# Kernel optimization log

Hardware: AMD Instinct MI355X
Metric: run time of the kernel (lower is better)

## Reference

```python
import jax, jax.numpy as jnp
import numpy as np

B, CIN, HID, T, W, H, TAU = 8, 16, 64, 4, 32, 32, 5
EPS = 1e-5
DN = ('NCDHW', 'OIDHW', 'NCDHW')


def conv3d(x, w, b):
    # 'same' conv3d, NCDHW layout
    y = jax.lax.conv_general_dilated(x, w, (1, 1, 1), 'SAME', dimension_numbers=DN)
    return y + b[None, :, None, None, None]


def ln3(u):
    # F.layer_norm over the last 3 (spatial) dims, no affine
    mu = jnp.mean(u, axis=(-3, -2, -1), keepdims=True)
    var = jnp.var(u, axis=(-3, -2, -1), keepdims=True)
    return (u - mu) * jax.lax.rsqrt(var + EPS)


def ln4(u, w, b):
    # nn.LayerNorm(memory_shape): over last 4 dims (C,T,W,H), with affine
    mu = jnp.mean(u, axis=(-4, -3, -2, -1), keepdims=True)
    var = jnp.var(u, axis=(-4, -3, -2, -1), keepdims=True)
    return (u - mu) * jax.lax.rsqrt(var + EPS) * w + b


def self_attention(r, c_history):
    scale = 1.0 / np.sqrt(T * W * H)
    scores = jnp.einsum('bctwh,lbctwh->bl', r, c_history) * scale  # [B, TAU]
    # faithful to source: softmax over dim=0 (the batch axis of the [b,l] scores)
    attn = jax.nn.softmax(scores, axis=0)
    return jnp.einsum('bl,lbctwh->bctwh', attn, c_history)


def setup_inputs() -> dict:
    key = jax.random.key(0)
    ks = jax.random.split(key, 8)
    x = jax.random.normal(ks[0], (B, CIN, T, W, H), jnp.float32)
    c_history = jax.random.normal(ks[1], (TAU, B, HID, T, W, H), jnp.float32)
    m = jax.random.normal(ks[2], (B, HID, T, W, H), jnp.float32)
    h = jax.random.normal(ks[3], (B, HID, T, W, H), jnp.float32)
    Wx = jax.random.normal(ks[4], (7, HID, CIN, 3, 3, 3), jnp.float32) * 0.05
    bx = jnp.zeros((7, HID), jnp.float32)
    # 9 state-branch conv kernels: [hr, hi, hg, mi', mg', mf', ho, co, mo]
    Wh = jax.random.normal(ks[5], (9, HID, HID, 3, 3, 3), jnp.float32) * 0.02
    bh = jnp.zeros((9, HID), jnp.float32)
    w111 = jax.random.normal(ks[6], (HID, 2 * HID, 1, 1, 1), jnp.float32) * 0.05
    b111 = jnp.zeros((HID,), jnp.float32)
    ln_w = jnp.ones((HID, T, W, H), jnp.float32)
    ln_b = jnp.zeros((HID, T, W, H), jnp.float32)
    return dict(x=x, c_history=c_history, m=m, h=h, Wx=Wx, bx=bx, Wh=Wh, bh=bh,
                w111=w111, b111=b111, ln_w=ln_w, ln_b=ln_b)


def reference(x, c_history, m, h, Wx, bx, Wh, bh, w111, b111, ln_w, ln_b):
    cx = lambda i: conv3d(x, Wx[i], bx[i])
    cs = lambda u, i: conv3d(u, Wh[i], bh[i])
    r = jax.nn.sigmoid(ln3(cx(0) + cs(h, 0)))
    i = jax.nn.sigmoid(ln3(cx(1) + cs(h, 1)))
    g = jnp.tanh(ln3(cx(2) + cs(h, 2)))
    recall = self_attention(r, c_history)
    c = i * g + ln4(c_history[-1] + recall, ln_w, ln_b)
    i_p = jax.nn.sigmoid(ln3(cx(3) + cs(m, 3)))
    g_p = jnp.tanh(ln3(cx(4) + cs(m, 4)))
    f_p = jax.nn.sigmoid(ln3(cx(5) + cs(m, 5)))
    m_new = i_p * g_p + f_p * m
    o = jax.nn.sigmoid(ln3(cx(6) + cs(h, 6) + cs(c, 7) + cs(m_new, 8)))
    h_new = o * jnp.tanh(conv3d(jnp.concatenate([c, m_new], axis=1), w111, b111))
    c_history_new = jnp.concatenate([c_history[1:], c[None]], axis=0)
    return (c_history_new, m_new, h_new)
```

## Files before the change

### kernel.cpp

```cpp
#include <hip/hip_runtime.h>
#include <hip/hip_bf16.h>
#include <math.h>

#define BATCH 8
#define CIN 16
#define HID 64
#define S2 1024
#define SP 4096
#define CHB 262144
#define TAU 5
#define GATE_SZ 2097152
#define EPS 1e-5f

#define WS_Z_OFF   ((size_t)3 * GATE_SZ)
#define WS_ST_OFF  ((size_t)4 * GATE_SZ)

typedef unsigned short u16;
typedef __attribute__((ext_vector_type(8))) short  short8;
typedef __attribute__((ext_vector_type(8))) u16    ushort8;
typedef __attribute__((ext_vector_type(4))) float  f32x4;

#define N7 (7*27*64*96)
#define NO (27*64*128)
#define N1 (64*128)

__device__ __forceinline__ u16 f2b(float v) {
    __hip_bfloat16 h = __float2bfloat16(v);
    u16 r; __builtin_memcpy(&r, &h, 2); return r;
}

__device__ __forceinline__ float* gate_ptr(float* out, float* ws, int g) {
    return (g < 4) ? (out + (size_t)g * GATE_SZ) : (ws + (size_t)(g - 4) * GATE_SZ);
}

__device__ __forceinline__ float fsig(float v) {
    v = fminf(fmaxf(v, -30.f), 30.f);
    return 1.f / (1.f + __expf(-v));
}
__device__ __forceinline__ float ftanh(float v) {
    v = fminf(fmaxf(v, -15.f), 15.f);
    const float t = __expf(-2.f * v);
    return (1.f - t) / (1.f + t);
}

__global__ __launch_bounds__(256) void pack_w_k(const float* __restrict__ Wx,
                                                const float* __restrict__ Wh,
                                                const float* __restrict__ w111,
                                                u16* __restrict__ A7, u16* __restrict__ Ao,
                                                u16* __restrict__ A111,
                                                float* __restrict__ stats,
                                                float* __restrict__ sums)
{
    const int idx = blockIdx.x * 256 + threadIdx.x;
    if (idx < 128)  stats[idx] = 0.f;
    if (idx < 6144) sums[idx] = 0.f;
    if (idx < N7) {
        const int k = idx % 96, oc = (idx / 96) % 64, tap = (idx / (96*64)) % 27, g = idx / (96*64*27);
        float v = 0.f;
        if (k < 16)      v = Wx[((size_t)(g*64 + oc)*16 + k)      * 27 + tap];
        else if (k < 80) v = Wh[((size_t)(g*64 + oc)*64 + (k-16)) * 27 + tap];
        A7[idx] = f2b(v);
    } else if (idx < N7 + NO) {
        const int j = idx - N7;
        const int k = j % 128, oc = (j / 128) % 64, tap = j / (128*64);
        float v = (k < 64) ? Wh[((size_t)(7*64 + oc)*64 + k)      * 27 + tap]
                           : Wh[((size_t)(8*64 + oc)*64 + (k-64)) * 27 + tap];
        Ao[j] = f2b(v);
    } else if (idx < N7 + NO + N1) {
        const int j = idx - N7 - NO;
        A111[j] = f2b(w111[j]);
    }
}

__global__ __launch_bounds__(256) void pack_xhm_k(const float* __restrict__ x,
                                                  const float* __restrict__ h,
                                                  const float* __restrict__ m,
                                                  u16* __restrict__ XH, u16* __restrict__ XM)
{
    __shared__ float t[144][65];
    const int bi = blockIdx.x, b = bi >> 6, s0 = (bi & 63) << 6;
    for (int i = threadIdx.x; i < 144*64; i += 256) {
        const int row = i >> 6, sc = i & 63;
        float v;
        if (row < 16)      v = x[((size_t)b*16 + row)      * SP + s0 + sc];
        else if (row < 80) v = h[((size_t)b*64 + (row-16)) * SP + s0 + sc];
        else               v = m[((size_t)b*64 + (row-80)) * SP + s0 + sc];
        t[row][sc] = v;
    }
    __syncthreads();
    for (int j = threadIdx.x; j < 64*96; j += 256) {
        const int s = j / 96, ch = j % 96;
        const size_t o = ((size_t)b*4096 + s0 + s) * 96 + ch;
        XH[o] = f2b(ch < 80 ? t[ch][s] : 0.f);
        XM[o] = f2b(ch < 16 ? t[ch][s] : (ch < 80 ? t[ch + 64][s] : 0.f));
    }
}

__device__ __forceinline__ int swz32(int r, int c) {
    return r * 32 + ((c ^ ((r >> 1) & 3)) << 3);
}

template<int KCH, int TAPS, int NR, int MODE, int MT, int MINW>
__global__ __launch_bounds__(256, MINW) void conv_mfma_k(
    const u16* __restrict__ XA, const u16* __restrict__ XB,
    const u16* __restrict__ Apack,
    const float* __restrict__ bxp, const float* __restrict__ bhp,
    const float* __restrict__ b111,
    float* __restrict__ out, float* __restrict__ ws,
    float* __restrict__ sums)
{
    constexpr int YT   = NR + 2;
    constexpr int ROWS = 4 * YT * 34;
    __shared__ __align__(16) u16 xs[ROWS * 32];

    const int bi = blockIdx.x;
    int g = 0, b, y0, ocb = 0, kc_lo = 0, kc_hi = KCH / 32;
    const u16* X; const u16* Ag; float* outp;
    if (MODE == 0) {
        constexpr int YB = 32 / NR;
        ocb = (bi & 1) * 32;
        const int r2 = bi >> 1;
        g  = r2 / (8 * YB);
        b  = (r2 / YB) % 8;
        y0 = (r2 % YB) * NR;
        X  = (g >= 3 && g <= 5) ? XB : XA;
        Ag = Apack + (size_t)g * TAPS * 64 * KCH;
        outp = gate_ptr(out, ws, g) + (size_t)b * CHB;
    } else if (MODE == 1) {
        b = bi >> 5; y0 = bi & 31;
        X = XA; Ag = Apack;
        outp = ws + (size_t)2 * GATE_SZ + (size_t)b * CHB;
    } else {
        b = bi >> 5; y0 = bi & 31;
        X = XA; Ag = Apack;
        outp = ws + (size_t)b * CHB;
    }
    const u16* Xb = X + (size_t)b * 4096 * KCH;

    const int tid  = threadIdx.x;
    const int w    = tid >> 6;
    const int lane = tid & 63;
    const int xn   = lane & 15, quad = lane >> 4;

    f32x4 acc[MT][2 * NR] = {};

    for (int kc = kc_lo; kc < kc_hi; ++kc) {
        if (kc != kc_lo) __syncthreads();
        for (int cix = tid; cix < ROWS * 4; cix += 256) {
            const int r = cix >> 2, sub = cix & 3;
            const int t = r / (YT * 34), rem = r % (YT * 34);
            const int yy = rem / 34, xx = rem % 34;
            const int gy = y0 + yy - 1, gx = xx - 1;
            ushort8 v = {0, 0, 0, 0, 0, 0, 0, 0};
            if ((unsigned)gy < 32u && (unsigned)gx < 32u)
                v = *(const ushort8*)&Xb[(size_t)(t * 1024 + gy * 32 + gx) * KCH + kc * 32 + sub * 8];
            *(ushort8*)&xs[swz32(r, sub)] = v;
        }
        __syncthreads();

        auto load_ab = [&](short8* a, short8* bf, int kd_, int ky_, int kx_) {
            const int tap = (TAPS == 27) ? (kd_ * 9 + ky_ * 3 + kx_) : 0;
            #pragma unroll
            for (int mt = 0; mt < MT; ++mt)
                a[mt] = *(const short8*)
                    &Ag[(size_t)(tap * 64 + ocb + mt * 16 + xn) * KCH + kc * 32 + quad * 8];
            const int rowt = (w + kd_ - 1) * YT * 34;
            #pragma unroll
            for (int nt = 0; nt < 2 * NR; ++nt) {
                const int ysub = nt >> 1, xh = nt & 1;
                const int row = rowt + (ysub + ky_) * 34 + xh * 16 + xn + kx_;
                bf[nt] = *(const short8*)&xs[swz32(row, quad)];
            }
        };
        auto do_mfma = [&](short8* a, short8* bf) {
            #pragma unroll
            for (int nt = 0; nt < 2 * NR; ++nt)
                #pragma unroll
                for (int mt = 0; mt < MT; ++mt)
                    acc[mt][nt] = __builtin_amdgcn_mfma_f32_16x16x32_bf16(a[mt], bf[nt], acc[mt][nt], 0, 0, 0);
        };

        if (TAPS == 27) {
            int kd = (w == 0) ? 1 : 0;
            const int kd_hi = (w == 3) ? 2 : 3;
            const int ntap = (kd_hi - kd) * 9;
            int ky = 0, kx = 0;
            auto adv = [&]() { if (++kx == 3) { kx = 0; if (++ky == 3) { ky = 0; ++kd; } } };

            short8 a0[MT], b0[2 * NR], a1[MT], b1[2 * NR];
            load_ab(a0, b0, kd, ky, kx);
            for (int t = 0; t + 2 <= ntap; t += 2) {
                adv(); load_ab(a1, b1, kd, ky, kx);
                do_mfma(a0, b0);
                if (t + 3 <= ntap) { adv(); load_ab(a0, b0, kd, ky, kx); }
                do_mfma(a1, b1);
            }
            if (ntap & 1) do_mfma(a0, b0);
        } else {
            short8 a0[MT], b0[2 * NR];
            load_ab(a0, b0, 1, 1, 1);
            do_mfma(a0, b0);
        }
    }

    #pragma unroll
    for (int mt = 0; mt < MT; ++mt)
    #pragma unroll
    for (int nt = 0; nt < 2 * NR; ++nt) {
        const int ysub = nt >> 1, xh = nt & 1;
        const int sp = w * 1024 + (y0 + ysub) * 32 + xh * 16 + xn;
        #pragma unroll
        for (int reg = 0; reg < 4; ++reg) {
            const int oc = ocb + mt * 16 + quad * 4 + reg;
            float bias;
            if (MODE == 0)      bias = bxp[g * 64 + oc] + bhp[g * 64 + oc];
            else if (MODE == 1) bias = bhp[7 * 64 + oc] + bhp[8 * 64 + oc];
            else                bias = b111[oc];
            float* p = outp + (size_t)oc * SP + sp;
            float vv = acc[mt][nt][reg] + bias;
            if (MODE == 1) vv += *p;
            *p = vv;
        }
    }

    if (MODE == 0 && g < 6) {
        #pragma unroll
        for (int mt = 0; mt < MT; ++mt)
        #pragma unroll
        for (int reg = 0; reg < 4; ++reg) {
            const int oc = ocb + mt * 16 + quad * 4 + reg;
            const float bias = bxp[g * 64 + oc] + bhp[g * 64 + oc];
            float s = 0.f, s2 = 0.f;
            #pragma unroll
            for (int nt = 0; nt < 2 * NR; ++nt) {
                const float vv = acc[mt][nt][reg] + bias;
                s += vv; s2 += vv * vv;
            }
            #pragma unroll
            for (int off = 8; off > 0; off >>= 1) {
                s  += __shfl_xor(s, off);
                s2 += __shfl_xor(s2, off);
            }
            if (xn == 0) {
                float* dst = &sums[(size_t)((g * 8 + b) * 64 + oc) * 2];
                atomicAdd(dst, s);
                atomicAdd(dst + 1, s2);
            }
        }
    }
}

__global__ __launch_bounds__(256) void ln3_act_k(float* __restrict__ out,
                                                 float* __restrict__ ws, int gate0)
{
    const int blk = blockIdx.x;
    const int g = gate0 + (blk >> 9);
    float* p = gate_ptr(out, ws, g) + (size_t)(blk & 511) * SP;
    const int tid = threadIdx.x;

    float s = 0.f, s2 = 0.f;
    for (int k = tid; k < SP; k += 256) { float v = p[k]; s += v; s2 += v * v; }
    #pragma unroll
    for (int off = 32; off > 0; off >>= 1) { s += __shfl_down(s, off); s2 += __shfl_down(s2, off); }
    __shared__ float rs[4], rs2[4], stat[2];
    if ((tid & 63) == 0) { rs[tid >> 6] = s; rs2[tid >> 6] = s2; }
    __syncthreads();
    if (tid == 0) {
        float S  = rs[0] + rs[1] + rs[2] + rs[3];
        float Sq = rs2[0] + rs2[1] + rs2[2] + rs2[3];
        float mu  = S * (1.f / SP);
        float var = Sq * (1.f / SP) - mu * mu;
        stat[0] = mu; stat[1] = rsqrtf(var + EPS);
    }
    __syncthreads();
    const float mu = stat[0], r = stat[1];
    for (int k = tid; k < SP; k += 256)
        p[k] = fsig((p[k] - mu) * r);
}

__global__ __launch_bounds__(256) void scores_k(const float* __restrict__ u0,
                                                const float* __restrict__ chist,
                                                const float* __restrict__ sums,
                                                float* __restrict__ stats)
{
    const int blk = blockIdx.x;
    const int b = blk >> 6, chn = blk & 63;
    const float* sp2 = &sums[(size_t)(b * 64 + chn) * 2];
    const float mu = sp2[0] * (1.f / SP);
    const float var = sp2[1] * (1.f / SP) - mu * mu;
    const float rr = rsqrtf(var + EPS);
    const float* rp = u0 + (size_t)b * CHB;
    const int lo = chn * SP;
    float s[TAU] = {};
    for (int k = lo + threadIdx.x; k < lo + SP; k += 256) {
        const float rv = fsig((rp[k] - mu) * rr);
        #pragma unroll
        for (int l = 0; l < TAU; ++l) s[l] += rv * chist[(size_t)(l * BATCH + b) * CHB + k];
    }
    __shared__ float rsh[TAU][4];
    #pragma unroll
    for (int l = 0; l < TAU; ++l) {
        float v = s[l];
        #pragma unroll
        for (int off = 32; off > 0; off >>= 1) v += __shfl_down(v, off);
        if ((threadIdx.x & 63) == 0) rsh[l][threadIdx.x >> 6] = v;
    }
    __syncthreads();
    if (threadIdx.x < TAU) {
        const int l = threadIdx.x;
        atomicAdd(&stats[l * 8 + b],
                  (rsh[l][0] + rsh[l][1] + rsh[l][2] + rsh[l][3]) * (1.f / 64.f));
    }
}

__global__ __launch_bounds__(256) void recall_k(const float* __restrict__ chist,
                                                float* __restrict__ ws,
                                                float* __restrict__ part)
{
    const float* stats = ws + WS_ST_OFF;
    const int blk = blockIdx.x;
    const int b = blk >> 10;
    const int idx = (blk & 1023) * 256 + threadIdx.x;

    __shared__ float attn[TAU];
    if (threadIdx.x < TAU) {
        const int l = threadIdx.x;
        float mx = -1e30f;
        for (int bb = 0; bb < BATCH; ++bb) mx = fmaxf(mx, stats[l * 8 + bb]);
        float sum = 0.f, e = 0.f;
        for (int bb = 0; bb < BATCH; ++bb) {
            float t = __expf(stats[l * 8 + bb] - mx);
            sum += t;
            if (bb == b) e = t;
        }
        attn[l] = e / sum;
    }
    __syncthreads();
    const float a0 = attn[0], a1 = attn[1], a2 = attn[2], a3 = attn[3], a4 = attn[4];

    const size_t e = (size_t)b * CHB + idx;
    const size_t LB = (size_t)BATCH * CHB;
    float z = chist[4 * LB + e] * (1.f + a4)
            + a0 * chist[0 * LB + e] + a1 * chist[1 * LB + e]
            + a2 * chist[2 * LB + e] + a3 * chist[3 * LB + e];
    ws[WS_Z_OFF + e] = z;

    float s = z, s2 = z * z;
    #pragma unroll
    for (int off = 32; off > 0; off >>= 1) { s += __shfl_down(s, off); s2 += __shfl_down(s2, off); }
    __shared__ float rs[4], rs2[4];
    if ((threadIdx.x & 63) == 0) { rs[threadIdx.x >> 6] = s; rs2[threadIdx.x >> 6] = s2; }
    __syncthreads();
    if (threadIdx.x == 0) {
        part[blk]        = rs[0] + rs[1] + rs[2] + rs[3];
        part[8192 + blk] = rs2[0] + rs2[1] + rs2[2] + rs2[3];
    }
}

__global__ __launch_bounds__(256) void cm_pcm_k(float* __restrict__ out, float* __restrict__ ws,
                                                const float* __restrict__ m,
                                                const float* __restrict__ lnw,
                                                const float* __restrict__ lnb,
                                                const float* __restrict__ part,
                                                const float* __restrict__ sums,
                                                u16* __restrict__ PCM)
{
    __shared__ __align__(16) u16 tl[64][136];
    __shared__ float lst[5][64][2];
    const int bi = blockIdx.x;
    const int b = bi >> 6;
    const int s0 = (bi & 63) << 6;

    for (int j = threadIdx.x; j < 5 * 64; j += 256) {
        const int gg = j >> 6, chn = j & 63;
        const float* sp2 = &sums[(size_t)(((gg + 1) * 8 + b) * 64 + chn) * 2];
        const float mu_ = sp2[0] * (1.f / SP);
        const float var_ = sp2[1] * (1.f / SP) - mu_ * mu_;
        lst[gg][chn][0] = mu_;
        lst[gg][chn][1] = rsqrtf(var_ + EPS);
    }
    float s = 0.f, s2 = 0.f;
    for (int j = threadIdx.x; j < 1024; j += 256) {
        s  += part[b * 1024 + j];
        s2 += part[8192 + b * 1024 + j];
    }
    #pragma unroll
    for (int off = 32; off > 0; off >>= 1) { s += __shfl_down(s, off); s2 += __shfl_down(s2, off); }
    __shared__ float rs[4], rs2[4], st[2];
    if ((threadIdx.x & 63) == 0) { rs[threadIdx.x >> 6] = s; rs2[threadIdx.x >> 6] = s2; }
    __syncthreads();
    if (threadIdx.x == 0) {
        float S  = rs[0] + rs[1] + rs[2] + rs[3];
        float Sq = rs2[0] + rs2[1] + rs2[2] + rs2[3];
        float mu  = S * (1.f / CHB);
        float var = Sq * (1.f / CHB) - mu * mu;
        st[0] = mu; st[1] = rsqrtf(var + EPS);
    }
    __syncthreads();
    const float mu = st[0], rstd = st[1];

    for (int i = threadIdx.x; i < 1024; i += 256) {
        const int chn = i >> 4;
        const int sp4 = (i & 15) << 2;
        const size_t e = (size_t)b * CHB + (size_t)chn * SP + s0 + sp4;
        const size_t le = (size_t)chn * SP + s0 + sp4;
        float4 z  = *(const float4*)&ws[WS_Z_OFF + e];
        float4 u1 = *(const float4*)&gate_ptr(out, ws, 1)[e];
        float4 u2 = *(const float4*)&gate_ptr(out, ws, 2)[e];
        float4 u3 = *(const float4*)&gate_ptr(out, ws, 3)[e];
        float4 u4 = *(const float4*)&gate_ptr(out, ws, 4)[e];
        float4 u5 = *(const float4*)&gate_ptr(out, ws, 5)[e];
        float4 mm = *(const float4*)&m[e];
        float4 lw = *(const float4*)&lnw[le];
        float4 lb = *(const float4*)&lnb[le];
        const float m1 = lst[0][chn][0], r1 = lst[0][chn][1];
        const float m2 = lst[1][chn][0], r2 = lst[1][chn][1];
        const float m3 = lst[2][chn][0], r3 = lst[2][chn][1];
        const float m4 = lst[3][chn][0], r4 = lst[3][chn][1];
        const float m5 = lst[4][chn][0], r5 = lst[4][chn][1];
        float4 c, mn;
        {
            const float uu1[4] = {u1.x, u1.y, u1.z, u1.w};
            const float uu2[4] = {u2.x, u2.y, u2.z, u2.w};
            const float uu3[4] = {u3.x, u3.y, u3.z, u3.w};
            const float uu4[4] = {u4.x, u4.y, u4.z, u4.w};
            const float uu5[4] = {u5.x, u5.y, u5.z, u5.w};
            const float zz[4]  = {z.x, z.y, z.z, z.w};
            const float mmv[4] = {mm.x, mm.y, mm.z, mm.w};
            const float lwv[4] = {lw.x, lw.y, lw.z, lw.w};
            const float lbv[4] = {lb.x, lb.y, lb.z, lb.w};
            float cv[4], mv[4];
            #pragma unroll
            for (int k = 0; k < 4; ++k) {
                const float gi = fsig ((uu1[k] - m1) * r1);
                const float gg = ftanh((uu2[k] - m2) * r2);
                const float ip = fsig ((uu3[k] - m3) * r3);
                const float gp = ftanh((uu4[k] - m4) * r4);
                const float fp = fsig ((uu5[k] - m5) * r5);
                cv[k] = gi * gg + (zz[k] - mu) * rstd * lwv[k] + lbv[k];
                mv[k] = ip * gp + fp * mmv[k];
                tl[sp4 + k][chn]      = f2b(cv[k]);
                tl[sp4 + k][64 + chn] = f2b(mv[k]);
            }
            c.x = cv[0]; c.y = cv[1]; c.z = cv[2]; c.w = cv[3];
            mn.x = mv[0]; mn.y = mv[1]; mn.z = mv[2]; mn.w = mv[3];
        }
        *(float4*)&out[(size_t)4 * GATE_SZ + e] = c;
        *(float4*)&out[(size_t)5 * GATE_SZ + e] = mn;
    }
    __syncthreads();
    for (int j = threadIdx.x; j < 1024; j += 256) {
        const int sidx = j >> 4, c8 = (j & 15) << 3;
        ushort8 v = *(const ushort8*)&tl[sidx][c8];
        *(ushort8*)&PCM[((size_t)b * 4096 + s0 + sidx) * 128 + c8] = v;
    }
}

__global__ __launch_bounds__(256) void tail_k(const float* __restrict__ chist,
                                              const float* __restrict__ o,
                                              const float* __restrict__ v,
                                              float* __restrict__ out)
{
    const int bi = blockIdx.x;
    if (bi < 8192) {
        const size_t i = (size_t)bi * 256 + threadIdx.x;
        ((float4*)out)[i] = ((const float4*)(chist + GATE_SZ))[i];
    } else {
        const size_t i = (size_t)(bi - 8192) * 256 + threadIdx.x;
        float4 ov = ((const float4*)o)[i], vv = ((const float4*)v)[i];
        float4 r;
        r.x = ov.x * ftanh(vv.x); r.y = ov.y * ftanh(vv.y);
        r.z = ov.z * ftanh(vv.z); r.w = ov.w * ftanh(vv.w);
        ((float4*)(out + (size_t)6 * GATE_SZ))[i] = r;
    }
}

extern "C" void kernel_launch(void* const* d_in, const int* in_sizes, int n_in,
                              void* d_out, int out_size, void* d_ws, size_t ws_size,
                              hipStream_t stream)
{
    const float* x    = (const float*)d_in[0];
    const float* ch   = (const float*)d_in[1];
    const float* m    = (const float*)d_in[2];
    const float* h    = (const float*)d_in[3];
    const float* Wx   = (const float*)d_in[4];
    const float* bx   = (const float*)d_in[5];
    const float* Wh   = (const float*)d_in[6];
    const float* bh   = (const float*)d_in[7];
    const float* w111 = (const float*)d_in[8];
    const float* b111 = (const float*)d_in[9];
    const float* lnw  = (const float*)d_in[10];
    const float* lnb  = (const float*)d_in[11];
    float* out = (float*)d_out;
    float* ws  = (float*)d_ws;

    u16* XH   = (u16*)(out + (size_t)4 * GATE_SZ);
    u16* A7   = (u16*)(out + (size_t)5 * GATE_SZ);
    u16* XM   = (u16*)(out + (size_t)6 * GATE_SZ);
    u16* Ao   = XM + (size_t)BATCH * 4096 * 96;
    u16* A111 = Ao + (size_t)NO;
    u16* PCM  = (u16*)out;
    float* part = (float*)(A111 + N1);
    float* sums = part + 16384;
    float* stats = ws + WS_ST_OFF;

    pack_w_k<<<(N7 + NO + N1 + 255) / 256, 256, 0, stream>>>(Wx, Wh, w111, A7, Ao, A111, stats, sums);
    pack_xhm_k<<<512, 256, 0, stream>>>(x, h, m, XH, XM);

    conv_mfma_k<96, 27, 2, 0, 2, 4><<<1792, 256, 0, stream>>>(XH, XM, A7, bx, bh, nullptr, out, ws, sums);

    scores_k<<<512, 256, 0, stream>>>(out, ch, sums, stats);
    recall_k<<<8192, 256, 0, stream>>>(ch, ws, part);
    cm_pcm_k<<<512, 256, 0, stream>>>(out, ws, m, lnw, lnb, part, sums, PCM);

    conv_mfma_k<128, 27, 1, 1, 4, 3><<<256, 256, 0, stream>>>(PCM, nullptr, Ao, nullptr, bh, nullptr, out, ws, nullptr);
    ln3_act_k<<<512, 256, 0, stream>>>(out, ws, 6);
    conv_mfma_k<128, 1, 1, 2, 4, 3><<<256, 256, 0, stream>>>(PCM, nullptr, A111, nullptr, nullptr, b111, out, ws, nullptr);

    tail_k<<<10240, 256, 0, stream>>>(ch, ws + (size_t)2 * GATE_SZ, ws, out);
}
```

Measured before the change: 402.7 us.

## Retile conv kernels: full 64-channel tiles for gate conv, split channels for o-conv

The first gate conv now has each block compute all 64 output channels (MT=4) across 896 blocks instead of splitting channels into two halves over 1792 blocks. This reuses each staged input tile in LDS across twice as many MFMAs and halves redundant input staging. The o-gate conv goes the other way: it splits channels (MT=2) across 512 blocks to get more parallelism. The software-pipelined double-buffered tap loop is replaced by a simple fully unrolled kd/jj loop, which leaves load/MFMA overlap to the compiler and may raise register pressure at MT=4.

```diff
diff --git a/kernel.cpp b/kernel.cpp
--- a/kernel.cpp
+++ b/kernel.cpp
@@ -118,16 +118,19 @@
     const u16* X; const u16* Ag; float* outp;
     if (MODE == 0) {
         constexpr int YB = 32 / NR;
-        ocb = (bi & 1) * 32;
-        const int r2 = bi >> 1;
-        g  = r2 / (8 * YB);
-        b  = (r2 / YB) % 8;
-        y0 = (r2 % YB) * NR;
+        if (MT == 2) {
+            ocb = (bi & 1) * 32;
+            const int r2 = bi >> 1;
+            g = r2 / (8 * YB); b = (r2 / YB) % 8; y0 = (r2 % YB) * NR;
+        } else {
+            g = bi / (8 * YB); b = (bi / YB) % 8; y0 = (bi % YB) * NR;
+        }
         X  = (g >= 3 && g <= 5) ? XB : XA;
         Ag = Apack + (size_t)g * TAPS * 64 * KCH;
         outp = gate_ptr(out, ws, g) + (size_t)b * CHB;
     } else if (MODE == 1) {
-        b = bi >> 5; y0 = bi & 31;
+        if (MT == 2) { ocb = (bi & 1) * 32; b = bi >> 6; y0 = (bi >> 1) & 31; }
+        else         { b = bi >> 5; y0 = bi & 31; }
         X = XA; Ag = Apack;
         outp = ws + (size_t)2 * GATE_SZ + (size_t)b * CHB;
     } else {
@@ -158,48 +161,48 @@
         }
         __syncthreads();
 
-        auto load_ab = [&](short8* a, short8* bf, int kd_, int ky_, int kx_) {
-            const int tap = (TAPS == 27) ? (kd_ * 9 + ky_ * 3 + kx_) : 0;
+        if (TAPS == 27) {
+            const int kd_lo = (w == 0) ? 1 : 0;
+            const int kd_hi = (w == 3) ? 2 : 3;
+            for (int kd = kd_lo; kd < kd_hi; ++kd) {
+                const int rowt = (w + kd - 1) * YT * 34;
+                #pragma unroll
+                for (int jj = 0; jj < 9; ++jj) {
+                    const int ky = jj / 3, kx = jj % 3;
+                    short8 a[MT], bf[2 * NR];
+                    #pragma unroll
+                    for (int mt = 0; mt < MT; ++mt)
+                        a[mt] = *(const short8*)
+                            &Ag[(size_t)((kd * 9 + jj) * 64 + ocb + mt * 16 + xn) * KCH + kc * 32 + quad * 8];
+                    #pragma unroll
+                    for (int nt = 0; nt < 2 * NR; ++nt) {
+                        const int ysub = nt >> 1, xh = nt & 1;
+                        const int row = rowt + (ysub + ky) * 34 + xh * 16 + xn + kx;
+                        bf[nt] = *(const short8*)&xs[swz32(row, quad)];
+                    }
+                    #pragma unroll
+                    for (int nt = 0; nt < 2 * NR; ++nt)
+                        #pragma unroll
+                        for (int mt = 0; mt < MT; ++mt)
+                            acc[mt][nt] = __builtin_amdgcn_mfma_f32_16x16x32_bf16(a[mt], bf[nt], acc[mt][nt], 0, 0, 0);
+                }
+            }
+        } else {
+            short8 a[MT], bf[2 * NR];
             #pragma unroll
             for (int mt = 0; mt < MT; ++mt)
-                a[mt] = *(const short8*)
-                    &Ag[(size_t)(tap * 64 + ocb + mt * 16 + xn) * KCH + kc * 32 + quad * 8];
-            const int rowt = (w + kd_ - 1) * YT * 34;
+                a[mt] = *(const short8*)&Ag[(size_t)(ocb + mt * 16 + xn) * KCH + kc * 32 + quad * 8];
             #pragma unroll
             for (int nt = 0; nt < 2 * NR; ++nt) {
                 const int ysub = nt >> 1, xh = nt & 1;
-                const int row = rowt + (ysub + ky_) * 34 + xh * 16 + xn + kx_;
+                const int row = (w * YT + ysub + 1) * 34 + xh * 16 + xn + 1;
                 bf[nt] = *(const short8*)&xs[swz32(row, quad)];
             }
-        };
-        auto do_mfma = [&](short8* a, short8* bf) {
             #pragma unroll
             for (int nt = 0; nt < 2 * NR; ++nt)
                 #pragma unroll
                 for (int mt = 0; mt < MT; ++mt)
                     acc[mt][nt] = __builtin_amdgcn_mfma_f32_16x16x32_bf16(a[mt], bf[nt], acc[mt][nt], 0, 0, 0);
-        };
-
-        if (TAPS == 27) {
-            int kd = (w == 0) ? 1 : 0;
-            const int kd_hi = (w == 3) ? 2 : 3;
-            const int ntap = (kd_hi - kd) * 9;
-            int ky = 0, kx = 0;
-            auto adv = [&]() { if (++kx == 3) { kx = 0; if (++ky == 3) { ky = 0; ++kd; } } };
-
-            short8 a0[MT], b0[2 * NR], a1[MT], b1[2 * NR];
-            load_ab(a0, b0, kd, ky, kx);
-            for (int t = 0; t + 2 <= ntap; t += 2) {
-                adv(); load_ab(a1, b1, kd, ky, kx);
-                do_mfma(a0, b0);
-                if (t + 3 <= ntap) { adv(); load_ab(a0, b0, kd, ky, kx); }
-                do_mfma(a1, b1);
-            }
-            if (ntap & 1) do_mfma(a0, b0);
-        } else {
-            short8 a0[MT], b0[2 * NR];
-            load_ab(a0, b0, 1, 1, 1);
-            do_mfma(a0, b0);
         }
     }
 
@@ -507,13 +510,13 @@
     pack_w_k<<<(N7 + NO + N1 + 255) / 256, 256, 0, stream>>>(Wx, Wh, w111, A7, Ao, A111, stats, sums);
     pack_xhm_k<<<512, 256, 0, stream>>>(x, h, m, XH, XM);
 
-    conv_mfma_k<96, 27, 2, 0, 2, 4><<<1792, 256, 0, stream>>>(XH, XM, A7, bx, bh, nullptr, out, ws, sums);
+    conv_mfma_k<96, 27, 2, 0, 4, 3><<<896, 256, 0, stream>>>(XH, XM, A7, bx, bh, nullptr, out, ws, sums);
 
     scores_k<<<512, 256, 0, stream>>>(out, ch, sums, stats);
     recall_k<<<8192, 256, 0, stream>>>(ch, ws, part);
     cm_pcm_k<<<512, 256, 0, stream>>>(out, ws, m, lnw, lnb, part, sums, PCM);
 
-    conv_mfma_k<128, 27, 1, 1, 4, 3><<<256, 256, 0, stream>>>(PCM, nullptr, Ao, nullptr, bh, nullptr, out, ws, nullptr);
+    conv_mfma_k<128, 27, 1, 1, 2, 4><<<512, 256, 0, stream>>>(PCM, nullptr, Ao, nullptr, bh, nullptr, out, ws, nullptr);
     ln3_act_k<<<512, 256, 0, stream>>>(out, ws, 6);
     conv_mfma_k<128, 1, 1, 2, 4, 3><<<256, 256, 0, stream>>>(PCM, nullptr, A111, nullptr, nullptr, b111, out, ws, nullptr);
 
```

After: 440.3 us. +9.3%, slower.

## Fuse o-gate layernorm stats into conv epilogue and sigmoid into tail kernel

Applied to the files above, without the earlier changes.

The o-gate conv now accumulates per-channel sum and sum-of-squares through atomics in its epilogue. The separate ln3_act pass is removed, and the normalisation plus sigmoid are applied inside tail_k. The shared-memory XOR swizzle is replaced by padding rows to 40 elements. The output-channel split moves from the first gate conv (now MT=4, 896 blocks) to the o-gate conv (MT=2, 512 blocks). This removes a full read-modify-write pass over one gate tensor and rebalances occupancy between the two convs, at the cost of more atomics and different LDS bank behaviour.

```diff
diff --git a/kernel.cpp b/kernel.cpp
--- a/kernel.cpp
+++ b/kernel.cpp
@@ -53,7 +53,7 @@
 {
     const int idx = blockIdx.x * 256 + threadIdx.x;
     if (idx < 128)  stats[idx] = 0.f;
-    if (idx < 6144) sums[idx] = 0.f;
+    if (idx < 7168) sums[idx] = 0.f;
     if (idx < N7) {
         const int k = idx % 96, oc = (idx / 96) % 64, tap = (idx / (96*64)) % 27, g = idx / (96*64*27);
         float v = 0.f;
@@ -96,10 +96,6 @@
     }
 }
 
-__device__ __forceinline__ int swz32(int r, int c) {
-    return r * 32 + ((c ^ ((r >> 1) & 3)) << 3);
-}
-
 template<int KCH, int TAPS, int NR, int MODE, int MT, int MINW>
 __global__ __launch_bounds__(256, MINW) void conv_mfma_k(
     const u16* __restrict__ XA, const u16* __restrict__ XB,
@@ -111,23 +107,24 @@
 {
     constexpr int YT   = NR + 2;
     constexpr int ROWS = 4 * YT * 34;
-    __shared__ __align__(16) u16 xs[ROWS * 32];
+    constexpr int PADK = 40;
+    __shared__ __align__(16) u16 xs[ROWS * PADK];
 
     const int bi = blockIdx.x;
-    int g = 0, b, y0, ocb = 0, kc_lo = 0, kc_hi = KCH / 32;
+    int g = 0, b, y0, ocb = 0;
     const u16* X; const u16* Ag; float* outp;
     if (MODE == 0) {
         constexpr int YB = 32 / NR;
-        ocb = (bi & 1) * 32;
-        const int r2 = bi >> 1;
-        g  = r2 / (8 * YB);
-        b  = (r2 / YB) % 8;
-        y0 = (r2 % YB) * NR;
+        g  = bi / (8 * YB);
+        b  = (bi / YB) % 8;
+        y0 = (bi % YB) * NR;
         X  = (g >= 3 && g <= 5) ? XB : XA;
         Ag = Apack + (size_t)g * TAPS * 64 * KCH;
         outp = gate_ptr(out, ws, g) + (size_t)b * CHB;
     } else if (MODE == 1) {
-        b = bi >> 5; y0 = bi & 31;
+        ocb = (bi & 1) * 32;
+        b  = bi >> 6;
+        y0 = (bi >> 1) & 31;
         X = XA; Ag = Apack;
         outp = ws + (size_t)2 * GATE_SZ + (size_t)b * CHB;
     } else {
@@ -144,8 +141,8 @@
 
     f32x4 acc[MT][2 * NR] = {};
 
-    for (int kc = kc_lo; kc < kc_hi; ++kc) {
-        if (kc != kc_lo) __syncthreads();
+    for (int kc = 0; kc < KCH / 32; ++kc) {
+        if (kc != 0) __syncthreads();
         for (int cix = tid; cix < ROWS * 4; cix += 256) {
             const int r = cix >> 2, sub = cix & 3;
             const int t = r / (YT * 34), rem = r % (YT * 34);
@@ -154,22 +151,26 @@
             ushort8 v = {0, 0, 0, 0, 0, 0, 0, 0};
             if ((unsigned)gy < 32u && (unsigned)gx < 32u)
                 v = *(const ushort8*)&Xb[(size_t)(t * 1024 + gy * 32 + gx) * KCH + kc * 32 + sub * 8];
-            *(ushort8*)&xs[swz32(r, sub)] = v;
+            *(ushort8*)&xs[r * PADK + sub * 8] = v;
         }
         __syncthreads();
 
-        auto load_ab = [&](short8* a, short8* bf, int kd_, int ky_, int kx_) {
-            const int tap = (TAPS == 27) ? (kd_ * 9 + ky_ * 3 + kx_) : 0;
+        auto load_a = [&](short8* a, int tap) {
             #pragma unroll
             for (int mt = 0; mt < MT; ++mt)
                 a[mt] = *(const short8*)
                     &Ag[(size_t)(tap * 64 + ocb + mt * 16 + xn) * KCH + kc * 32 + quad * 8];
-            const int rowt = (w + kd_ - 1) * YT * 34;
+        };
+        auto load_b = [&](short8* bf, int tap) {
+            int kd, ky, kx;
+            if (TAPS == 27) { kd = tap / 9; ky = (tap / 3) % 3; kx = tap % 3; }
+            else            { kd = 1; ky = 1; kx = 1; }
+            const int tin = w + kd - 1;
             #pragma unroll
             for (int nt = 0; nt < 2 * NR; ++nt) {
                 const int ysub = nt >> 1, xh = nt & 1;
-                const int row = rowt + (ysub + ky_) * 34 + xh * 16 + xn + kx_;
-                bf[nt] = *(const short8*)&xs[swz32(row, quad)];
+                bf[nt] = *(const short8*)
+                    &xs[((tin * YT + ysub + ky) * 34 + xh * 16 + xn + kx) * PADK + quad * 8];
             }
         };
         auto do_mfma = [&](short8* a, short8* bf) {
@@ -181,101 +182,60 @@
         };
 
         if (TAPS == 27) {
-            int kd = (w == 0) ? 1 : 0;
-            const int kd_hi = (w == 3) ? 2 : 3;
-            const int ntap = (kd_hi - kd) * 9;
-            int ky = 0, kx = 0;
-            auto adv = [&]() { if (++kx == 3) { kx = 0; if (++ky == 3) { ky = 0; ++kd; } } };
-
+            const int tap_lo = (w == 0) ? 9 : 0;
+            const int tap_hi = (w == 3) ? 18 : 27;
             short8 a0[MT], b0[2 * NR], a1[MT], b1[2 * NR];
-            load_ab(a0, b0, kd, ky, kx);
-            for (int t = 0; t + 2 <= ntap; t += 2) {
-                adv(); load_ab(a1, b1, kd, ky, kx);
+            load_a(a0, tap_lo); load_b(b0, tap_lo);
+            int tap = tap_lo;
+            for (; tap + 2 <= tap_hi; tap += 2) {
+                load_a(a1, tap + 1); load_b(b1, tap + 1);
                 do_mfma(a0, b0);
-                if (t + 3 <= ntap) { adv(); load_ab(a0, b0, kd, ky, kx); }
+                if (tap + 2 < tap_hi) { load_a(a0, tap + 2); load_b(b0, tap + 2); }
                 do_mfma(a1, b1);
             }
-            if (ntap & 1) do_mfma(a0, b0);
+            if (tap < tap_hi) do_mfma(a0, b0);
         } else {
             short8 a0[MT], b0[2 * NR];
-            load_ab(a0, b0, 1, 1, 1);
+            load_a(a0, 0); load_b(b0, 0);
             do_mfma(a0, b0);
         }
     }
 
+    constexpr bool SUMS1 = (MODE == 1);
     #pragma unroll
     for (int mt = 0; mt < MT; ++mt)
     #pragma unroll
-    for (int nt = 0; nt < 2 * NR; ++nt) {
-        const int ysub = nt >> 1, xh = nt & 1;
-        const int sp = w * 1024 + (y0 + ysub) * 32 + xh * 16 + xn;
+    for (int reg = 0; reg < 4; ++reg) {
+        const int oc = ocb + mt * 16 + quad * 4 + reg;
+        float bias;
+        if (MODE == 0)      bias = bxp[g * 64 + oc] + bhp[g * 64 + oc];
+        else if (MODE == 1) bias = bhp[7 * 64 + oc] + bhp[8 * 64 + oc];
+        else                bias = b111[oc];
+        float s = 0.f, s2 = 0.f;
         #pragma unroll
-        for (int reg = 0; reg < 4; ++reg) {
-            const int oc = ocb + mt * 16 + quad * 4 + reg;
-            float bias;
-            if (MODE == 0)      bias = bxp[g * 64 + oc] + bhp[g * 64 + oc];
-            else if (MODE == 1) bias = bhp[7 * 64 + oc] + bhp[8 * 64 + oc];
-            else                bias = b111[oc];
+        for (int nt = 0; nt < 2 * NR; ++nt) {
+            const int ysub = nt >> 1, xh = nt & 1;
+            const int sp = w * 1024 + (y0 + ysub) * 32 + xh * 16 + xn;
             float* p = outp + (size_t)oc * SP + sp;
             float vv = acc[mt][nt][reg] + bias;
             if (MODE == 1) vv += *p;
             *p = vv;
-        }
-    }
-
-    if (MODE == 0 && g < 6) {
-        #pragma unroll
-        for (int mt = 0; mt < MT; ++mt)
-        #pragma unroll
-        for (int reg = 0; reg < 4; ++reg) {
-            const int oc = ocb + mt * 16 + quad * 4 + reg;
-            const float bias = bxp[g * 64 + oc] + bhp[g * 64 + oc];
-            float s = 0.f, s2 = 0.f;
-            #pragma unroll
-            for (int nt = 0; nt < 2 * NR; ++nt) {
-                const float vv = acc[mt][nt][reg] + bias;
-                s += vv; s2 += vv * vv;
-            }
+            s += vv; s2 += vv * vv;
+        }
+        if ((MODE == 0 && g < 6) || SUMS1) {
             #pragma unroll
             for (int off = 8; off > 0; off >>= 1) {
                 s  += __shfl_xor(s, off);
                 s2 += __shfl_xor(s2, off);
             }
             if (xn == 0) {
-                float* dst = &sums[(size_t)((g * 8 + b) * 64 + oc) * 2];
+                const int gs = SUMS1 ? 6 : g;
+                float* dst = &sums[(size_t)((gs * 8 + b) * 64 + oc) * 2];
                 atomicAdd(dst, s);
                 atomicAdd(dst + 1, s2);
             }
         }
     }
-}
-
-__global__ __launch_bounds__(256) void ln3_act_k(float* __restrict__ out,
-                                                 float* __restrict__ ws, int gate0)
-{
-    const int blk = blockIdx.x;
-    const int g = gate0 + (blk >> 9);
-    float* p = gate_ptr(out, ws, g) + (size_t)(blk & 511) * SP;
-    const int tid = threadIdx.x;
-
-    float s = 0.f, s2 = 0.f;
-    for (int k = tid; k < SP; k += 256) { float v = p[k]; s += v; s2 += v * v; }
-    #pragma unroll
-    for (int off = 32; off > 0; off >>= 1) { s += __shfl_down(s, off); s2 += __shfl_down(s2, off); }
-    __shared__ float rs[4], rs2[4], stat[2];
-    if ((tid & 63) == 0) { rs[tid >> 6] = s; rs2[tid >> 6] = s2; }
-    __syncthreads();
-    if (tid == 0) {
-        float S  = rs[0] + rs[1] + rs[2] + rs[3];
-        float Sq = rs2[0] + rs2[1] + rs2[2] + rs2[3];
-        float mu  = S * (1.f / SP);
-        float var = Sq * (1.f / SP) - mu * mu;
-        stat[0] = mu; stat[1] = rsqrtf(var + EPS);
-    }
-    __syncthreads();
-    const float mu = stat[0], r = stat[1];
-    for (int k = tid; k < SP; k += 256)
-        p[k] = fsig((p[k] - mu) * r);
 }
 
 __global__ __launch_bounds__(256) void scores_k(const float* __restrict__ u0,
@@ -457,8 +417,9 @@
 }
 
 __global__ __launch_bounds__(256) void tail_k(const float* __restrict__ chist,
-                                              const float* __restrict__ o,
+                                              const float* __restrict__ u6,
                                               const float* __restrict__ v,
+                                              const float* __restrict__ sums,
                                               float* __restrict__ out)
 {
     const int bi = blockIdx.x;
@@ -466,11 +427,21 @@
         const size_t i = (size_t)bi * 256 + threadIdx.x;
         ((float4*)out)[i] = ((const float4*)(chist + GATE_SZ))[i];
     } else {
-        const size_t i = (size_t)(bi - 8192) * 256 + threadIdx.x;
-        float4 ov = ((const float4*)o)[i], vv = ((const float4*)v)[i];
+        const int j = bi - 8192;
+        const size_t e0 = (size_t)j * 1024;
+        const int b   = (int)(e0 >> 18);
+        const int chn = (int)((e0 >> 12) & 63);
+        const float* sp2 = &sums[(size_t)((6 * 8 + b) * 64 + chn) * 2];
+        const float mu = sp2[0] * (1.f / SP);
+        const float var = sp2[1] * (1.f / SP) - mu * mu;
+        const float rr = rsqrtf(var + EPS);
+        const size_t i = (size_t)j * 256 + threadIdx.x;
+        float4 uv = ((const float4*)u6)[i], vv = ((const float4*)v)[i];
         float4 r;
-        r.x = ov.x * ftanh(vv.x); r.y = ov.y * ftanh(vv.y);
-        r.z = ov.z * ftanh(vv.z); r.w = ov.w * ftanh(vv.w);
+        r.x = fsig((uv.x - mu) * rr) * ftanh(vv.x);
+        r.y = fsig((uv.y - mu) * rr) * ftanh(vv.y);
+        r.z = fsig((uv.z - mu) * rr) * ftanh(vv.z);
+        r.w = fsig((uv.w - mu) * rr) * ftanh(vv.w);
         ((float4*)(out + (size_t)6 * GATE_SZ))[i] = r;
     }
 }
@@ -507,15 +478,14 @@
     pack_w_k<<<(N7 + NO + N1 + 255) / 256, 256, 0, stream>>>(Wx, Wh, w111, A7, Ao, A111, stats, sums);
     pack_xhm_k<<<512, 256, 0, stream>>>(x, h, m, XH, XM);
 
-    conv_mfma_k<96, 27, 2, 0, 2, 4><<<1792, 256, 0, stream>>>(XH, XM, A7, bx, bh, nullptr, out, ws, sums);
+    conv_mfma_k<96, 27, 2, 0, 4, 3><<<896, 256, 0, stream>>>(XH, XM, A7, bx, bh, nullptr, out, ws, sums);
 
     scores_k<<<512, 256, 0, stream>>>(out, ch, sums, stats);
     recall_k<<<8192, 256, 0, stream>>>(ch, ws, part);
     cm_pcm_k<<<512, 256, 0, stream>>>(out, ws, m, lnw, lnb, part, sums, PCM);
 
-    conv_mfma_k<128, 27, 1, 1, 4, 3><<<256, 256, 0, stream>>>(PCM, nullptr, Ao, nullptr, bh, nullptr, out, ws, nullptr);
-    ln3_act_k<<<512, 256, 0, stream>>>(out, ws, 6);
+    conv_mfma_k<128, 27, 1, 1, 2, 4><<<512, 256, 0, stream>>>(PCM, nullptr, Ao, nullptr, bh, nullptr, out, ws, sums);
     conv_mfma_k<128, 1, 1, 2, 4, 3><<<256, 256, 0, stream>>>(PCM, nullptr, A111, nullptr, nullptr, b111, out, ws, nullptr);
 
-    tail_k<<<10240, 256, 0, stream>>>(ch, ws + (size_t)2 * GATE_SZ, ws, out);
-}
+    tail_k<<<10240, 256, 0, stream>>>(ch, ws + (size_t)2 * GATE_SZ, ws, sums, out);
+}
```

New measurement: 408.4 us. About the same (+1.4%).
